# Optimization experiments

Measured on AMD Instinct MI355X. Metric: run time of the kernel, lower is better.

The kernel has to match this reference:

```python
import jax, jax.numpy as jnp
import numpy as np

N, T, D, H = 64, 512, 512, 512


def _xavier(key, shape):
    fan_in, fan_out = shape
    limit = float(np.sqrt(6.0 / (fan_in + fan_out)))
    return jax.random.uniform(key, shape, jnp.float32, -limit, limit)


def setup_inputs() -> dict:
    key = jax.random.key(0)
    ks = jax.random.split(key, 5)
    return {
        "x": jax.random.normal(ks[0], (N, T, D), jnp.float32),
        "W_x_fwd": _xavier(ks[1], (D, 3 * H)),
        "W_h_fwd": _xavier(ks[2], (H, 3 * H)),
        "b_fwd": jnp.zeros((3 * H,), jnp.float32),
        "W_x_bwd": _xavier(ks[3], (D, 3 * H)),
        "W_h_bwd": _xavier(ks[4], (H, 3 * H)),
        "b_bwd": jnp.zeros((3 * H,), jnp.float32),
    }


def _gru(x, W_x, W_h, b):
    # x: [N, T, D]; precompute input projection once (as the torch code does)
    xm = jnp.einsum("ntd,dh->nth", x, W_x)  # [N, T, 3H]
    b_z, b_r, b_g = jnp.split(b, 3)
    h0 = jnp.zeros((x.shape[0], W_h.shape[0]), x.dtype)

    def step(h_prev, xt):  # xt: [N, 3H]
        h_z, h_r, h_g = jnp.split(h_prev @ W_h, 3, axis=-1)
        x_z, x_r, x_g = jnp.split(xt, 3, axis=-1)
        zt = jax.nn.sigmoid(x_z + h_z + b_z)
        rt = jax.nn.sigmoid(x_r + h_r + b_r)
        gt = jnp.tanh(x_g + rt * h_g + b_g)
        h_t = (1 - zt) * gt + zt * h_prev
        return h_t, h_t

    _, hs = jax.lax.scan(step, h0, jnp.swapaxes(xm, 0, 1))  # hs: [T, N, H]
    return jnp.swapaxes(hs, 0, 1)  # [N, T, H]


def reference(x, W_x_fwd, W_h_fwd, b_fwd, W_x_bwd, W_h_bwd, b_bwd):
    h_fwd = _gru(x, W_x_fwd, W_h_fwd, b_fwd)
    h_bwd = _gru(jnp.flip(x, axis=1), W_x_bwd, W_h_bwd, b_bwd)
    h_bwd = jnp.flip(h_bwd, axis=1)
    return jnp.concatenate([h_fwd, h_bwd], axis=-1)  # [N, T, 2H]
```

## Files before the change

kernel.cpp:

```cpp
#include <hip/hip_runtime.h>
#include <stdint.h>

#define NN 64
#define TT 512
#define DD 512
#define HH 512
#define H3 1536
#define MROWS (NN * TT)

#define GRPN 4
#define CBLK 8
#define MN 16

typedef _Float16 f16;
typedef f16 f16x8 __attribute__((ext_vector_type(8)));
typedef float f32x4 __attribute__((ext_vector_type(4)));
typedef unsigned long long ull;

#define XM_BYTES    ((size_t)2 * TT * NN * H3 * 2)
#define WPACK_BYTES ((size_t)2 * CBLK * 8 * 3 * 8 * 64 * 8 * 2)
#define HBUF_BYTES  ((size_t)2 * 2 * GRPN * MN * 256 * 8)
#define CNT_BYTES   ((size_t)512)

__global__ void repack_wh_frag(const float* __restrict__ whf,
                               const float* __restrict__ whb,
                               f16* __restrict__ wpack) {
    const int cb = blockIdx.x;
    const int dir = blockIdx.y;
    const float* src = dir ? whb : whf;
    f16* dst = wpack + ((size_t)(dir * CBLK + cb)) * 12288 * 8;
    for (int c = threadIdx.x; c < 12288; c += blockDim.x) {
        const int lane = c & 63;
        const int ks = (c >> 6) & 7;
        const int q2 = c >> 9;
        const int t = q2 % 3;
        const int w = q2 / 3;
        const int k = (w >> 2) * 256 + ks * 32 + (lane >> 4) * 8;
        const int u = cb * 64 + (w & 3) * 16 + (lane & 15);
        const int gcol = t * 512 + u;
        f16x8 v;
        #pragma unroll
        for (int j = 0; j < 8; ++j)
            v[j] = (f16)src[(size_t)(k + j) * H3 + gcol];
        *(f16x8*)(dst + (size_t)c * 8) = v;
    }
}

__global__ __launch_bounds__(256, 2) void gemm_xw(const float* __restrict__ x,
                                                  const float* __restrict__ wxf,
                                                  const float* __restrict__ wxb,
                                                  f16* __restrict__ xm) {
    const int dir = blockIdx.z;
    const float* w = dir ? wxb : wxf;
    f16* out = xm + (size_t)dir * MROWS * H3;
    const int c0 = blockIdx.x * 128;
    const int r0 = blockIdx.y * 128;
    __shared__ float sA[32][128];
    __shared__ float sB[32][128];
    const int t = threadIdx.x;
    const int tx = t & 15, ty = t >> 4;
    float acc[8][8];
    #pragma unroll
    for (int i = 0; i < 8; ++i)
        #pragma unroll
        for (int j = 0; j < 8; ++j) acc[i][j] = 0.f;

    for (int k0 = 0; k0 < DD; k0 += 32) {
        #pragma unroll
        for (int i = 0; i < 4; ++i) {
            int idx = t * 4 + i;
            int m = idx >> 3;
            int c = idx & 7;
            float4 u = *(const float4*)(x + (size_t)(r0 + m) * DD + k0 + c * 4);
            sA[c * 4 + 0][m] = u.x;
            sA[c * 4 + 1][m] = u.y;
            sA[c * 4 + 2][m] = u.z;
            sA[c * 4 + 3][m] = u.w;
        }
        #pragma unroll
        for (int i = 0; i < 4; ++i) {
            int idx = t * 4 + i;
            int kk = idx >> 5;
            int ch = idx & 31;
            *(float4*)&sB[kk][ch * 4] =
                *(const float4*)(w + (size_t)(k0 + kk) * H3 + c0 + ch * 4);
        }
        __syncthreads();
        for (int k = 0; k < 32; ++k) {
            float4 a0 = *(const float4*)&sA[k][ty * 8];
            float4 a1 = *(const float4*)&sA[k][ty * 8 + 4];
            float4 b0 = *(const float4*)&sB[k][tx * 8];
            float4 b1 = *(const float4*)&sB[k][tx * 8 + 4];
            float a[8] = {a0.x, a0.y, a0.z, a0.w, a1.x, a1.y, a1.z, a1.w};
            float b[8] = {b0.x, b0.y, b0.z, b0.w, b1.x, b1.y, b1.z, b1.w};
            #pragma unroll
            for (int ii = 0; ii < 8; ++ii)
                #pragma unroll
                for (int jj = 0; jj < 8; ++jj)
                    acc[ii][jj] = fmaf(a[ii], b[jj], acc[ii][jj]);
        }
        __syncthreads();
    }
    #pragma unroll
    for (int ii = 0; ii < 8; ++ii) {
        const size_t r = (size_t)(r0 + ty * 8 + ii);
        const size_t tt = r & 511, n = r >> 9;
        f16x8 v;
        #pragma unroll
        for (int jj = 0; jj < 8; ++jj) v[jj] = (f16)acc[ii][jj];
        *(f16x8*)(out + (tt * 64 + n) * H3 + c0 + tx * 8) = v;
    }
}

__global__ __launch_bounds__(512, 1) void gru_scan_mfma(
        const f16* __restrict__ xm,
        const f16* __restrict__ wpack,
        const float* __restrict__ b_f, const float* __restrict__ b_b,
        ull* __restrict__ hbuf,
        unsigned int* __restrict__ flags,
        float* __restrict__ out) {
    const int cb  = blockIdx.x;
    const int g   = blockIdx.y;
    const int dir = blockIdx.z;
    const int tid = threadIdx.x;
    const int lane = tid & 63, wave = tid >> 6;
    const int kh = wave >> 2;
    const int ug = wave & 3;

    __shared__ __align__(16) unsigned char himg[16384];
    __shared__ float part[4][3][16][20];

    f16x8 bfrag[3][8];
    {
        const f16* wp = wpack +
            ((size_t)(dir * CBLK + cb) * 12288 + (size_t)wave * 1536) * 8;
        #pragma unroll
        for (int t = 0; t < 3; ++t)
            #pragma unroll
            for (int ks = 0; ks < 8; ++ks)
                bfrag[t][ks] = *(const f16x8*)(wp + ((size_t)((t * 8 + ks) * 64 + lane)) * 8);
    }

    const int u_l = cb * 64 + ug * 16 + (lane & 15);
    const int nrow0 = (lane >> 4) * 4;
    const float* bias = dir ? b_b : b_f;
    float bz = 0.f, br = 0.f, bg = 0.f;
    if (kh == 0) { bz = bias[u_l]; br = bias[512 + u_l]; bg = bias[1024 + u_l]; }
    const f16* xmd = xm + (size_t)dir * TT * NN * H3;
    unsigned int* rdg = flags + (dir * GRPN + g) * 16;

    const int fb = (lane & 15) * 1024 + kh * 512 + (lane >> 4) * 16;
    const int fswz = ((lane & 15) & 7) << 4;

    float hprev[4] = {0.f, 0.f, 0.f, 0.f};
    float px[3][4];
    float hnew[4];
    union H16 { f16 h; unsigned short u; };

    for (int s = 0; s < TT; ++s) {
        const int tc = dir ? (TT - 1 - s) : s;

        if (kh == 0) {
            #pragma unroll
            for (int r = 0; r < 4; ++r) {
                const int n = g * 16 + nrow0 + r;
                const size_t ro = ((size_t)tc * 64 + n) * H3 + u_l;
                px[0][r] = (float)xmd[ro];
                px[1][r] = (float)xmd[ro + 512];
                px[2][r] = (float)xmd[ro + 1024];
            }
        }

        {
            const ull* hr8 = hbuf +
                (((size_t)(s & 1) * 2 + dir) * GRPN + g) * 4096;
            ull tmp[8];
            #pragma unroll
            for (int i = 0; i < 8; ++i)
                tmp[i] = __hip_atomic_load(hr8 + i * 512 + tid,
                                           __ATOMIC_RELAXED, __HIP_MEMORY_SCOPE_AGENT);
            const unsigned int want = (unsigned int)s;
            for (;;) {
                bool bad = false;
                #pragma unroll
                for (int i = 0; i < 8; ++i)
                    bad |= ((unsigned int)(tmp[i] >> 32) < want);
                if (!__any(bad)) break;
                #pragma unroll
                for (int i = 0; i < 8; ++i)
                    if ((unsigned int)(tmp[i] >> 32) < want)
                        tmp[i] = __hip_atomic_load(hr8 + i * 512 + tid,
                                                   __ATOMIC_RELAXED, __HIP_MEMORY_SCOPE_AGENT);
                __builtin_amdgcn_s_sleep(1);
            }
            #pragma unroll
            for (int i = 0; i < 8; ++i) {
                const int off = (i * 512 + tid) * 4;
                const int row = off >> 10;
                *(unsigned int*)(himg + (off ^ ((row & 7) << 4))) =
                    (unsigned int)tmp[i];
            }
        }
        __syncthreads();

        if (tid == 0)
            __hip_atomic_store(&rdg[cb], (unsigned int)(s + 1),
                               __ATOMIC_RELAXED, __HIP_MEMORY_SCOPE_AGENT);

        f32x4 a0 = {0.f, 0.f, 0.f, 0.f};
        f32x4 a1 = {0.f, 0.f, 0.f, 0.f};
        f32x4 a2 = {0.f, 0.f, 0.f, 0.f};
        #pragma unroll
        for (int ks = 0; ks < 8; ++ks) {
            f16x8 av = *(const f16x8*)(himg + ((fb + ks * 64) ^ fswz));
            a0 = __builtin_amdgcn_mfma_f32_16x16x32_f16(av, bfrag[0][ks], a0, 0, 0, 0);
            a1 = __builtin_amdgcn_mfma_f32_16x16x32_f16(av, bfrag[1][ks], a1, 0, 0, 0);
            a2 = __builtin_amdgcn_mfma_f32_16x16x32_f16(av, bfrag[2][ks], a2, 0, 0, 0);
        }
        if (kh == 1) {
            #pragma unroll
            for (int r = 0; r < 4; ++r) {
                part[ug][0][nrow0 + r][lane & 15] = a0[r];
                part[ug][1][nrow0 + r][lane & 15] = a1[r];
                part[ug][2][nrow0 + r][lane & 15] = a2[r];
            }
        }
        __syncthreads();

        if (kh == 0) {
            #pragma unroll
            for (int r = 0; r < 4; ++r) {
                const float sz = px[0][r] + a0[r] + part[ug][0][nrow0 + r][lane & 15] + bz;
                const float sr = px[1][r] + a1[r] + part[ug][1][nrow0 + r][lane & 15] + br;
                const float hg = a2[r] + part[ug][2][nrow0 + r][lane & 15];
                const float z  = 1.f / (1.f + __expf(-sz));
                const float rr = 1.f / (1.f + __expf(-sr));
                const float gg = 1.f - 2.f / (1.f + __expf(2.f * (px[2][r] + rr * hg + bg)));
                hnew[r] = (1.f - z) * gg + z * hprev[r];
                hprev[r] = hnew[r];
            }
        } else if (wave == 4 && s > 0) {
            const unsigned int tgt = (unsigned int)s;
            while (true) {
                unsigned int v = __hip_atomic_load(&rdg[lane & 7],
                            __ATOMIC_RELAXED, __HIP_MEMORY_SCOPE_AGENT);
                if (__all(v >= tgt)) break;
                __builtin_amdgcn_s_sleep(1);
            }
        }
        __syncthreads();

        if (kh == 0) {
            #pragma unroll
            for (int r = 0; r < 4; ++r) {
                const int n = g * 16 + nrow0 + r;
                out[((size_t)n * TT + tc) * 1024 + dir * 512 + u_l] = hnew[r];
            }
            if (s < TT - 1) {
                ull* nslab = hbuf +
                    (((size_t)((s + 1) & 1) * 2 + dir) * GRPN + g) * 4096;
                #pragma unroll
                for (int r = 0; r < 4; ++r) {
                    H16 hx; hx.h = (f16)hnew[r];
                    const unsigned int ob = (unsigned int)__shfl_xor((int)hx.u, 1, 64);
                    if (!(lane & 1)) {
                        const ull pk = (ull)((unsigned int)hx.u | (ob << 16))
                                     | ((ull)(s + 1) << 32);
                        __hip_atomic_store(nslab + (nrow0 + r) * 256 + (u_l >> 1),
                                           pk, __ATOMIC_RELAXED, __HIP_MEMORY_SCOPE_AGENT);
                    }
                }
            }
        }
    }
}

__global__ __launch_bounds__(512) void gru_scan_fused(const float* __restrict__ x,
                                                      const float* __restrict__ wxf,
                                                      const float* __restrict__ whf,
                                                      const float* __restrict__ b_f,
                                                      const float* __restrict__ wxb,
                                                      const float* __restrict__ whb,
                                                      const float* __restrict__ b_b,
                                                      float* __restrict__ out) {
    const int n = blockIdx.x;
    const int dir = blockIdx.y;
    const int tid = threadIdx.x;
    const float* wx = dir ? wxb : wxf;
    const float* wh = dir ? whb : whf;
    const float* bias = dir ? b_b : b_f;
    const float bz = bias[tid];
    const float br = bias[512 + tid];
    const float bg = bias[1024 + tid];

    __shared__ float sh[512];
    __shared__ float shx[512];
    sh[tid] = 0.f;
    float hprev = 0.f;
    __syncthreads();

    for (int s = 0; s < TT; ++s) {
        const int tc = dir ? (TT - 1 - s) : s;
        shx[tid] = x[((size_t)n * TT + tc) * DD + tid];
        __syncthreads();
        float az = 0.f, ar = 0.f, ag = 0.f;
        float xz = 0.f, xr = 0.f, xg = 0.f;
        #pragma unroll 2
        for (int k = 0; k < DD; ++k) {
            const float hk = sh[k];
            const float xk = shx[k];
            const size_t rowb = (size_t)k * H3 + tid;
            az = fmaf(wh[rowb], hk, az);
            ar = fmaf(wh[rowb + 512], hk, ar);
            ag = fmaf(wh[rowb + 1024], hk, ag);
            xz = fmaf(wx[rowb], xk, xz);
            xr = fmaf(wx[rowb + 512], xk, xr);
            xg = fmaf(wx[rowb + 1024], xk, xg);
        }
        const float z = 1.f / (1.f + __expf(-(xz + az + bz)));
        const float r = 1.f / (1.f + __expf(-(xr + ar + br)));
        const float g = 1.f - 2.f / (1.f + __expf(2.f * (xg + r * ag + bg)));
        const float hnew = (1.f - z) * g + z * hprev;
        __syncthreads();
        sh[tid] = hnew;
        hprev = hnew;
        out[((size_t)n * TT + tc) * 1024 + (size_t)dir * 512 + tid] = hnew;
        __syncthreads();
    }
}

extern "C" void kernel_launch(void* const* d_in, const int* in_sizes, int n_in,
                              void* d_out, int out_size, void* d_ws, size_t ws_size,
                              hipStream_t stream) {
    const float* x   = (const float*)d_in[0];
    const float* wxf = (const float*)d_in[1];
    const float* whf = (const float*)d_in[2];
    const float* bf_ = (const float*)d_in[3];
    const float* wxb = (const float*)d_in[4];
    const float* whb = (const float*)d_in[5];
    const float* bb_ = (const float*)d_in[6];
    float* out = (float*)d_out;

    const size_t need = XM_BYTES + WPACK_BYTES + HBUF_BYTES + CNT_BYTES;

    if (ws_size >= need) {
        f16* xm = (f16*)d_ws;
        f16* wpack = (f16*)((char*)d_ws + XM_BYTES);
        ull* hbuf = (ull*)((char*)d_ws + XM_BYTES + WPACK_BYTES);
        unsigned int* flags = (unsigned int*)((char*)d_ws + XM_BYTES + WPACK_BYTES + HBUF_BYTES);
        hipMemsetAsync(hbuf, 0, HBUF_BYTES + CNT_BYTES, stream);
        repack_wh_frag<<<dim3(CBLK, 2), 256, 0, stream>>>(whf, whb, wpack);
        gemm_xw<<<dim3(12, 256, 2), 256, 0, stream>>>(x, wxf, wxb, xm);
        gru_scan_mfma<<<dim3(CBLK, GRPN, 2), 512, 0, stream>>>(xm, wpack, bf_, bb_,
                                                               hbuf, flags, out);
    } else {
        gru_scan_fused<<<dim3(64, 2), 512, 0, stream>>>(x, wxf, whf, bf_,
                                                        wxb, whb, bb_, out);
    }
}
```

Measured before the change: 3.331 ms.

## Add fast-path h exchange with sc0 loads, remap blocks, prefetch xm

Per-step hidden-state exchange now goes through a second buffer copy. That copy is read with sc0 global loads, which can hit in a nearer cache level, and the layout is changed so each thread reads 8 contiguous ull. The slow agent-scope atomic reload is used only every fourth poll round as a fallback. The grid is flattened so blocks sharing a direction and group are interleaved, which changes placement across XCDs. Next-step xm values are prefetched after the h publish, and the output store is moved after it, to shorten the critical path. Relying on sc0 loads for coherence across CUs risks reading stale data longer or incorrect visibility.

```diff
diff --git a/kernel.cpp b/kernel.cpp
--- a/kernel.cpp
+++ b/kernel.cpp
@@ -19,7 +19,8 @@
 
 #define XM_BYTES    ((size_t)2 * TT * NN * H3 * 2)
 #define WPACK_BYTES ((size_t)2 * CBLK * 8 * 3 * 8 * 64 * 8 * 2)
-#define HBUF_BYTES  ((size_t)2 * 2 * GRPN * MN * 256 * 8)
+#define FAST_OFF    ((size_t)2 * 2 * GRPN * 4096)
+#define HBUF_BYTES  (FAST_OFF * 8 * 2)
 #define CNT_BYTES   ((size_t)512)
 
 __global__ void repack_wh_frag(const float* __restrict__ whf,
@@ -112,6 +113,23 @@
     }
 }
 
+__device__ __forceinline__ void fast_ld8(const ull* a, ull (&t)[8]) {
+    asm volatile(
+        "global_load_dwordx2 %0, %8, off sc0\n\t"
+        "global_load_dwordx2 %1, %8, off offset:8 sc0\n\t"
+        "global_load_dwordx2 %2, %8, off offset:16 sc0\n\t"
+        "global_load_dwordx2 %3, %8, off offset:24 sc0\n\t"
+        "global_load_dwordx2 %4, %8, off offset:32 sc0\n\t"
+        "global_load_dwordx2 %5, %8, off offset:40 sc0\n\t"
+        "global_load_dwordx2 %6, %8, off offset:48 sc0\n\t"
+        "global_load_dwordx2 %7, %8, off offset:56 sc0\n\t"
+        "s_waitcnt vmcnt(0)"
+        : "=&v"(t[0]), "=&v"(t[1]), "=&v"(t[2]), "=&v"(t[3]),
+          "=&v"(t[4]), "=&v"(t[5]), "=&v"(t[6]), "=&v"(t[7])
+        : "v"(a)
+        : "memory");
+}
+
 __global__ __launch_bounds__(512, 1) void gru_scan_mfma(
         const f16* __restrict__ xm,
         const f16* __restrict__ wpack,
@@ -119,9 +137,10 @@
         ull* __restrict__ hbuf,
         unsigned int* __restrict__ flags,
         float* __restrict__ out) {
-    const int cb  = blockIdx.x;
-    const int g   = blockIdx.y;
-    const int dir = blockIdx.z;
+    const int groupid = blockIdx.x & 7;
+    const int cb      = blockIdx.x >> 3;
+    const int dir     = groupid & 1;
+    const int g       = groupid >> 1;
     const int tid = threadIdx.x;
     const int lane = tid & 63, wave = tid >> 6;
     const int kh = wave >> 2;
@@ -157,41 +176,50 @@
     float hnew[4];
     union H16 { f16 h; unsigned short u; };
 
+    if (kh == 0) {
+        const int tc0 = dir ? (TT - 1) : 0;
+        #pragma unroll
+        for (int r = 0; r < 4; ++r) {
+            const int n = g * 16 + nrow0 + r;
+            const size_t ro = ((size_t)tc0 * 64 + n) * H3 + u_l;
+            px[0][r] = (float)xmd[ro];
+            px[1][r] = (float)xmd[ro + 512];
+            px[2][r] = (float)xmd[ro + 1024];
+        }
+    }
+
     for (int s = 0; s < TT; ++s) {
         const int tc = dir ? (TT - 1 - s) : s;
 
-        if (kh == 0) {
-            #pragma unroll
-            for (int r = 0; r < 4; ++r) {
-                const int n = g * 16 + nrow0 + r;
-                const size_t ro = ((size_t)tc * 64 + n) * H3 + u_l;
-                px[0][r] = (float)xmd[ro];
-                px[1][r] = (float)xmd[ro + 512];
-                px[2][r] = (float)xmd[ro + 1024];
-            }
-        }
-
+        ull tmp[8];
         {
-            const ull* hr8 = hbuf +
-                (((size_t)(s & 1) * 2 + dir) * GRPN + g) * 4096;
-            ull tmp[8];
-            #pragma unroll
-            for (int i = 0; i < 8; ++i)
-                tmp[i] = __hip_atomic_load(hr8 + i * 512 + tid,
-                                           __ATOMIC_RELAXED, __HIP_MEMORY_SCOPE_AGENT);
+            const ull* sb8 = hbuf +
+                (((size_t)(s & 1) * 2 + dir) * GRPN + g) * 4096 + tid * 8;
+            const ull* fb8 = sb8 + FAST_OFF;
+            fast_ld8(fb8, tmp);
             const unsigned int want = (unsigned int)s;
+            int rounds = 0;
             for (;;) {
                 bool bad = false;
                 #pragma unroll
                 for (int i = 0; i < 8; ++i)
                     bad |= ((unsigned int)(tmp[i] >> 32) < want);
                 if (!__any(bad)) break;
-                #pragma unroll
-                for (int i = 0; i < 8; ++i)
-                    if ((unsigned int)(tmp[i] >> 32) < want)
-                        tmp[i] = __hip_atomic_load(hr8 + i * 512 + tid,
-                                                   __ATOMIC_RELAXED, __HIP_MEMORY_SCOPE_AGENT);
-                __builtin_amdgcn_s_sleep(1);
+                ++rounds;
+                if ((rounds & 3) == 0) {
+                    #pragma unroll
+                    for (int i = 0; i < 8; ++i)
+                        if ((unsigned int)(tmp[i] >> 32) < want)
+                            tmp[i] = __hip_atomic_load(sb8 + i,
+                                        __ATOMIC_RELAXED, __HIP_MEMORY_SCOPE_AGENT);
+                    __builtin_amdgcn_s_sleep(1);
+                } else {
+                    ull t2[8];
+                    fast_ld8(fb8, t2);
+                    #pragma unroll
+                    for (int i = 0; i < 8; ++i)
+                        if ((unsigned int)(tmp[i] >> 32) < want) tmp[i] = t2[i];
+                }
             }
             #pragma unroll
             for (int i = 0; i < 8; ++i) {
@@ -251,11 +279,6 @@
         __syncthreads();
 
         if (kh == 0) {
-            #pragma unroll
-            for (int r = 0; r < 4; ++r) {
-                const int n = g * 16 + nrow0 + r;
-                out[((size_t)n * TT + tc) * 1024 + dir * 512 + u_l] = hnew[r];
-            }
             if (s < TT - 1) {
                 ull* nslab = hbuf +
                     (((size_t)((s + 1) & 1) * 2 + dir) * GRPN + g) * 4096;
@@ -266,9 +289,30 @@
                     if (!(lane & 1)) {
                         const ull pk = (ull)((unsigned int)hx.u | (ob << 16))
                                      | ((ull)(s + 1) << 32);
-                        __hip_atomic_store(nslab + (nrow0 + r) * 256 + (u_l >> 1),
-                                           pk, __ATOMIC_RELAXED, __HIP_MEMORY_SCOPE_AGENT);
+                        const int sid = (nrow0 + r) * 256 + (u_l >> 1);
+                        ull* sa = nslab + (((sid & 511) << 3) + (sid >> 9));
+                        ull* fa = sa + FAST_OFF;
+                        asm volatile("global_store_dwordx2 %0, %1, off"
+                                     :: "v"(fa), "v"(pk) : "memory");
+                        __hip_atomic_store(sa, pk,
+                                __ATOMIC_RELAXED, __HIP_MEMORY_SCOPE_AGENT);
                     }
+                }
+            }
+            #pragma unroll
+            for (int r = 0; r < 4; ++r) {
+                const int n = g * 16 + nrow0 + r;
+                out[((size_t)n * TT + tc) * 1024 + dir * 512 + u_l] = hnew[r];
+            }
+            if (s < TT - 1) {
+                const int tcn = dir ? (TT - 2 - s) : (s + 1);
+                #pragma unroll
+                for (int r = 0; r < 4; ++r) {
+                    const int n = g * 16 + nrow0 + r;
+                    const size_t ro = ((size_t)tcn * 64 + n) * H3 + u_l;
+                    px[0][r] = (float)xmd[ro];
+                    px[1][r] = (float)xmd[ro + 512];
+                    px[2][r] = (float)xmd[ro + 1024];
                 }
             }
         }
@@ -351,8 +395,8 @@
         hipMemsetAsync(hbuf, 0, HBUF_BYTES + CNT_BYTES, stream);
         repack_wh_frag<<<dim3(CBLK, 2), 256, 0, stream>>>(whf, whb, wpack);
         gemm_xw<<<dim3(12, 256, 2), 256, 0, stream>>>(x, wxf, wxb, xm);
-        gru_scan_mfma<<<dim3(CBLK, GRPN, 2), 512, 0, stream>>>(xm, wpack, bf_, bb_,
-                                                               hbuf, flags, out);
+        gru_scan_mfma<<<dim3(64), 512, 0, stream>>>(xm, wpack, bf_, bb_,
+                                                    hbuf, flags, out);
     } else {
         gru_scan_fused<<<dim3(64, 2), 512, 0, stream>>>(x, wxf, whf, bf_,
                                                         wxb, whb, bb_, out);
```

New measurement: 3.859 ms. 1.16x slower.

## Use 4-deep h ring buffer, double-buffered LDS, and remove one barrier per step

Applied to the files above, without the earlier changes.

The state exchange buffer grows to a 4-slot ring, and the LDS h image is double-buffered. This lets the reader-readiness wait move off the critical path: it now checks readiness from two steps back in a separate wave, and the third __syncthreads per step is dropped. The next step's xm input is prefetched after the gate math, and the h slab layout is rearranged so each thread reads 8 contiguous words. Spin sleeps apply only after several polling rounds, and block ids are remapped so the groups for one column block are adjacent. The relaxed ring protocol carries a correctness risk if the slack assumptions are wrong.

```diff
diff --git a/kernel.cpp b/kernel.cpp
--- a/kernel.cpp
+++ b/kernel.cpp
@@ -11,6 +11,7 @@
 #define GRPN 4
 #define CBLK 8
 #define MN 16
+#define RING 4
 
 typedef _Float16 f16;
 typedef f16 f16x8 __attribute__((ext_vector_type(8)));
@@ -19,7 +20,7 @@
 
 #define XM_BYTES    ((size_t)2 * TT * NN * H3 * 2)
 #define WPACK_BYTES ((size_t)2 * CBLK * 8 * 3 * 8 * 64 * 8 * 2)
-#define HBUF_BYTES  ((size_t)2 * 2 * GRPN * MN * 256 * 8)
+#define HBUF_BYTES  ((size_t)RING * 2 * GRPN * 4096 * 8)
 #define CNT_BYTES   ((size_t)512)
 
 __global__ void repack_wh_frag(const float* __restrict__ whf,
@@ -119,15 +120,16 @@
         ull* __restrict__ hbuf,
         unsigned int* __restrict__ flags,
         float* __restrict__ out) {
-    const int cb  = blockIdx.x;
-    const int g   = blockIdx.y;
-    const int dir = blockIdx.z;
+    const int groupid = blockIdx.x & 7;
+    const int cb      = blockIdx.x >> 3;
+    const int dir     = groupid & 1;
+    const int g       = groupid >> 1;
     const int tid = threadIdx.x;
     const int lane = tid & 63, wave = tid >> 6;
     const int kh = wave >> 2;
     const int ug = wave & 3;
 
-    __shared__ __align__(16) unsigned char himg[16384];
+    __shared__ __align__(16) unsigned char himg[2][16384];
     __shared__ float part[4][3][16][20];
 
     f16x8 bfrag[3][8];
@@ -157,47 +159,59 @@
     float hnew[4];
     union H16 { f16 h; unsigned short u; };
 
+    if (kh == 0) {
+        const int tc0 = dir ? (TT - 1) : 0;
+        #pragma unroll
+        for (int r = 0; r < 4; ++r) {
+            const int n = g * 16 + nrow0 + r;
+            const size_t ro = ((size_t)tc0 * 64 + n) * H3 + u_l;
+            px[0][r] = (float)xmd[ro];
+            px[1][r] = (float)xmd[ro + 512];
+            px[2][r] = (float)xmd[ro + 1024];
+        }
+    }
+
     for (int s = 0; s < TT; ++s) {
         const int tc = dir ? (TT - 1 - s) : s;
 
-        if (kh == 0) {
-            #pragma unroll
-            for (int r = 0; r < 4; ++r) {
-                const int n = g * 16 + nrow0 + r;
-                const size_t ro = ((size_t)tc * 64 + n) * H3 + u_l;
-                px[0][r] = (float)xmd[ro];
-                px[1][r] = (float)xmd[ro + 512];
-                px[2][r] = (float)xmd[ro + 1024];
+        if (wave == 7 && s >= 3 && s < TT - 1) {
+            const unsigned int tgt = (unsigned int)(s - 2);
+            for (;;) {
+                unsigned int v = __hip_atomic_load(&rdg[lane & 7],
+                            __ATOMIC_RELAXED, __HIP_MEMORY_SCOPE_AGENT);
+                if (__all(v >= tgt)) break;
+                __builtin_amdgcn_s_sleep(1);
             }
         }
 
         {
-            const ull* hr8 = hbuf +
-                (((size_t)(s & 1) * 2 + dir) * GRPN + g) * 4096;
+            const ull* sb8 = hbuf +
+                (((size_t)(s & 3) * 2 + dir) * GRPN + g) * 4096 + tid * 8;
             ull tmp[8];
             #pragma unroll
             for (int i = 0; i < 8; ++i)
-                tmp[i] = __hip_atomic_load(hr8 + i * 512 + tid,
+                tmp[i] = __hip_atomic_load(sb8 + i,
                                            __ATOMIC_RELAXED, __HIP_MEMORY_SCOPE_AGENT);
             const unsigned int want = (unsigned int)s;
+            int rounds = 0;
             for (;;) {
                 bool bad = false;
                 #pragma unroll
                 for (int i = 0; i < 8; ++i)
                     bad |= ((unsigned int)(tmp[i] >> 32) < want);
                 if (!__any(bad)) break;
+                if (++rounds > 8) __builtin_amdgcn_s_sleep(1);
                 #pragma unroll
                 for (int i = 0; i < 8; ++i)
                     if ((unsigned int)(tmp[i] >> 32) < want)
-                        tmp[i] = __hip_atomic_load(hr8 + i * 512 + tid,
-                                                   __ATOMIC_RELAXED, __HIP_MEMORY_SCOPE_AGENT);
-                __builtin_amdgcn_s_sleep(1);
+                        tmp[i] = __hip_atomic_load(sb8 + i,
+                                    __ATOMIC_RELAXED, __HIP_MEMORY_SCOPE_AGENT);
             }
             #pragma unroll
             for (int i = 0; i < 8; ++i) {
                 const int off = (i * 512 + tid) * 4;
                 const int row = off >> 10;
-                *(unsigned int*)(himg + (off ^ ((row & 7) << 4))) =
+                *(unsigned int*)(&himg[s & 1][off ^ ((row & 7) << 4)]) =
                     (unsigned int)tmp[i];
             }
         }
@@ -212,7 +226,7 @@
         f32x4 a2 = {0.f, 0.f, 0.f, 0.f};
         #pragma unroll
         for (int ks = 0; ks < 8; ++ks) {
-            f16x8 av = *(const f16x8*)(himg + ((fb + ks * 64) ^ fswz));
+            f16x8 av = *(const f16x8*)(&himg[s & 1][(fb + ks * 64) ^ fswz]);
             a0 = __builtin_amdgcn_mfma_f32_16x16x32_f16(av, bfrag[0][ks], a0, 0, 0, 0);
             a1 = __builtin_amdgcn_mfma_f32_16x16x32_f16(av, bfrag[1][ks], a1, 0, 0, 0);
             a2 = __builtin_amdgcn_mfma_f32_16x16x32_f16(av, bfrag[2][ks], a2, 0, 0, 0);
@@ -239,26 +253,9 @@
                 hnew[r] = (1.f - z) * gg + z * hprev[r];
                 hprev[r] = hnew[r];
             }
-        } else if (wave == 4 && s > 0) {
-            const unsigned int tgt = (unsigned int)s;
-            while (true) {
-                unsigned int v = __hip_atomic_load(&rdg[lane & 7],
-                            __ATOMIC_RELAXED, __HIP_MEMORY_SCOPE_AGENT);
-                if (__all(v >= tgt)) break;
-                __builtin_amdgcn_s_sleep(1);
-            }
-        }
-        __syncthreads();
-
-        if (kh == 0) {
-            #pragma unroll
-            for (int r = 0; r < 4; ++r) {
-                const int n = g * 16 + nrow0 + r;
-                out[((size_t)n * TT + tc) * 1024 + dir * 512 + u_l] = hnew[r];
-            }
             if (s < TT - 1) {
                 ull* nslab = hbuf +
-                    (((size_t)((s + 1) & 1) * 2 + dir) * GRPN + g) * 4096;
+                    (((size_t)((s + 1) & 3) * 2 + dir) * GRPN + g) * 4096;
                 #pragma unroll
                 for (int r = 0; r < 4; ++r) {
                     H16 hx; hx.h = (f16)hnew[r];
@@ -266,9 +263,26 @@
                     if (!(lane & 1)) {
                         const ull pk = (ull)((unsigned int)hx.u | (ob << 16))
                                      | ((ull)(s + 1) << 32);
-                        __hip_atomic_store(nslab + (nrow0 + r) * 256 + (u_l >> 1),
-                                           pk, __ATOMIC_RELAXED, __HIP_MEMORY_SCOPE_AGENT);
+                        const int sid = (nrow0 + r) * 256 + (u_l >> 1);
+                        __hip_atomic_store(nslab + (((sid & 511) << 3) + (sid >> 9)),
+                                pk, __ATOMIC_RELAXED, __HIP_MEMORY_SCOPE_AGENT);
                     }
+                }
+            }
+            #pragma unroll
+            for (int r = 0; r < 4; ++r) {
+                const int n = g * 16 + nrow0 + r;
+                out[((size_t)n * TT + tc) * 1024 + dir * 512 + u_l] = hnew[r];
+            }
+            if (s < TT - 1) {
+                const int tcn = dir ? (TT - 2 - s) : (s + 1);
+                #pragma unroll
+                for (int r = 0; r < 4; ++r) {
+                    const int n = g * 16 + nrow0 + r;
+                    const size_t ro = ((size_t)tcn * 64 + n) * H3 + u_l;
+                    px[0][r] = (float)xmd[ro];
+                    px[1][r] = (float)xmd[ro + 512];
+                    px[2][r] = (float)xmd[ro + 1024];
                 }
             }
         }
@@ -351,8 +365,8 @@
         hipMemsetAsync(hbuf, 0, HBUF_BYTES + CNT_BYTES, stream);
         repack_wh_frag<<<dim3(CBLK, 2), 256, 0, stream>>>(whf, whb, wpack);
         gemm_xw<<<dim3(12, 256, 2), 256, 0, stream>>>(x, wxf, wxb, xm);
-        gru_scan_mfma<<<dim3(CBLK, GRPN, 2), 512, 0, stream>>>(xm, wpack, bf_, bb_,
-                                                               hbuf, flags, out);
+        gru_scan_mfma<<<dim3(64), 512, 0, stream>>>(xm, wpack, bf_, bb_,
+                                                    hbuf, flags, out);
     } else {
         gru_scan_fused<<<dim3(64, 2), 512, 0, stream>>>(x, wxf, whf, bf_,
                                                         wxb, whb, bb_, out);
```

Result: slower. 4.095 ms (+22.9%).
